# Kernel optimization log

Hardware: AMD Instinct MI355X
Metric: run time of the kernel (lower is better)

## Reference

```python
import jax, jax.numpy as jnp
import numpy as np

B, N, L, H = 32, 1024, 512, 8  # batch, num_id, Input_len, num_head
EPS = 1e-5


def _ln(x, g, b):
    m = jnp.mean(x, axis=-1, keepdims=True)
    v = jnp.mean((x - m) ** 2, axis=-1, keepdims=True)
    return (x - m) / jnp.sqrt(v + EPS) * g + b


def setup_inputs() -> dict:
    key = jax.random.key(0)
    ks = iter(jax.random.split(key, 40))
    w = lambda shape, s=0.02: jax.random.normal(next(ks), shape, jnp.float32) * s
    inp = {"x": jax.random.normal(next(ks), (B, N, L), jnp.float32)}
    for p in ("t", "c"):  # Time_de_att and cross_de_att params (conv1d k=1 -> [L,L])
        inp[f"{p}_Wq"] = w((L, L)); inp[f"{p}_bq"] = w((L,))
        inp[f"{p}_Wk"] = w((L, L)); inp[f"{p}_bk"] = w((L,))
        inp[f"{p}_Wv"] = w((L, L)); inp[f"{p}_bv"] = w((L,))
        inp[f"{p}_Wo"] = w((L, L, 1, H)); inp[f"{p}_bo"] = w((L,))  # Conv2d kernel (1,H)
        inp[f"{p}_g"] = jnp.ones((L,), jnp.float32); inp[f"{p}_b"] = jnp.zeros((L,), jnp.float32)
    inp["s_Wq"] = w((N, N)); inp["s_bq"] = w((N,))
    inp["s_Wk"] = w((N, N)); inp["s_bk"] = w((N,))
    inp["s_Wv"] = w((N, N)); inp["s_bv"] = w((N,))
    inp["s_W1"] = w((1, H)); inp["s_b1"] = w((1,))
    return inp


def _conv1x1(x_cn, W, b):  # x_cn: [B,C,len], W: [O,C]
    return jnp.einsum('oc,bcn->bon', W, x_cn) + b[None, :, None]


def _de_att(xq_src, xkv_src, Wq, bq, Wk, bk, Wv, bv, Wo, bo, g, bt):
    # xq_src, xkv_src: [B,L,N] (channels-first, as after x.transpose(-2,-1))
    q = _conv1x1(xq_src, Wq, bq).transpose(0, 2, 1)   # [B,N,L]
    k = _conv1x1(xkv_src, Wk, bk)                     # [B,L,N]
    v = _conv1x1(xkv_src, Wv, bv).transpose(0, 2, 1)  # [B,N,L]
    kd = jnp.sqrt(jnp.float32(N) / H)                 # k.shape[-1] == num_id
    attn = jax.nn.softmax(jnp.matmul(q, k) / kd, axis=-1)  # [B,N,N]
    line = jnp.matmul(attn, v)                        # [B,N,L]
    # eval-mode: all heads identical -> Conv2d(1,H) combine == sum weights over head axis
    Wsum = Wo[:, :, 0, :].sum(-1)                     # [L,L]
    res = jnp.einsum('oc,bcn->bon', Wsum, line.transpose(0, 2, 1)) + bo[None, :, None]
    out = (xkv_src + res).transpose(0, 2, 1)          # [B,N,L]
    return _ln(out, g, bt)


def reference(x,
              t_Wq, t_bq, t_Wk, t_bk, t_Wv, t_bv, t_Wo, t_bo, t_g, t_b,
              c_Wq, c_bq, c_Wk, c_bk, c_Wv, c_bv, c_Wo, c_bo, c_g, c_b,
              s_Wq, s_bq, s_Wk, s_bk, s_Wv, s_bv, s_W1, s_b1):
    xt = x.transpose(0, 2, 1)  # [B,L,N]
    # Time_de_att (self-attention over nodes, time as channels)
    time_out = _de_att(xt, xt, t_Wq, t_bq, t_Wk, t_bk, t_Wv, t_bv, t_Wo, t_bo, t_g, t_b)  # [B,N,L]
    # space_att2 (attention over time, nodes as features)
    q = xt @ s_Wq.T + s_bq                          # [B,L,N]
    k = (xt @ s_Wk.T + s_bk).transpose(0, 2, 1)     # [B,N,L]
    v = xt @ s_Wv.T + s_bv                          # [B,L,N]
    kd = jnp.sqrt(jnp.float32(L) / H)               # k.shape[-1] == Input_len
    line = jnp.matmul(jax.nn.softmax(jnp.matmul(q, k) / kd, axis=-1), v)  # [B,L,N]
    space_out = (line * s_W1.sum() + s_b1[0]).transpose(0, 2, 1)          # [B,N,L]
    # cross_de_att: q from space_out, k/v + residual from time_out
    out = _de_att(space_out.transpose(0, 2, 1), time_out.transpose(0, 2, 1),
                  c_Wq, c_bq, c_Wk, c_bk, c_Wv, c_bv, c_Wo, c_bo, c_g, c_b)
    return out  # [B,N,L]
```

## Files before the change

kernel.cpp:

```cpp
#include <hip/hip_runtime.h>
#include <hip/hip_bf16.h>

typedef __bf16 bf16;
typedef __bf16 bf16x8 __attribute__((ext_vector_type(8)));
typedef __bf16 bf16x4 __attribute__((ext_vector_type(4)));
typedef __bf16 bf16x2 __attribute__((ext_vector_type(2)));
typedef float f32x4 __attribute__((ext_vector_type(4)));

#define BATCH 32
#define N_ID 1024
#define L_IN 512

static const long ACT_E = (long)BATCH * N_ID * L_IN;
static const long S_NL  = (long)N_ID * L_IN;
static const long S_TT  = (long)N_ID * N_ID;

__device__ __forceinline__ void gload16(const bf16* g, bf16* l)
{
    __builtin_amdgcn_global_load_lds((__attribute__((address_space(1))) void*)g,
                                     (__attribute__((address_space(3))) void*)l, 16, 0, 0);
}

#define VM3 asm volatile("s_waitcnt vmcnt(3)" ::: "memory")
#define VM9 asm volatile("s_waitcnt vmcnt(9)" ::: "memory")
#define VM0 asm volatile("s_waitcnt vmcnt(0)" ::: "memory")
#define BAR __builtin_amdgcn_s_barrier()

#define COMPUTE(CIDX) \
    { \
      const bf16* pa = ldsb + (CIDX) * 12288; \
      const bf16* pb = pa + 8192; \
      bf16x8 af[4], bfv[4]; \
_Pragma("unroll") \
      for (int i = 0; i < 4; ++i) \
        af[i] = *(const bf16x8*)(pa + (wm * 64 + i * 16 + fr) * 32 + slotk); \
_Pragma("unroll") \
      for (int j = 0; j < 4; ++j) \
        bfv[j] = *(const bf16x8*)(pb + (wn * 64 + j * 16 + fr) * 32 + slotk); \
      __builtin_amdgcn_s_setprio(1); \
_Pragma("unroll") \
      for (int i = 0; i < 4; ++i) \
_Pragma("unroll") \
        for (int j = 0; j < 4; ++j) \
          acc[i][j] = __builtin_amdgcn_mfma_f32_16x16x32_bf16(af[i], bfv[j], acc[i][j], 0, 0, 0); \
      __builtin_amdgcn_s_setprio(0); \
    }

#define STAGE(CIDX, KT) { stgA(ldsb + (CIDX) * 12288, KT); \
                          stgB(ldsb + (CIDX) * 12288 + 8192, KT); }

template<int EPI>
__global__ __launch_bounds__(512, 4)
void gemm3(const bf16* __restrict__ A, const bf16* __restrict__ Bm, void* __restrict__ Cout,
           const float* __restrict__ biasCol, const float* __restrict__ biasRow,
           const void* __restrict__ Res, const float* __restrict__ scal2,
           float scale, int K,
           long lda, long ldb, long ldc,
           long sA, long sB, long sC, long sRes, long sBR, long sVp, int nsl,
           unsigned gy, unsigned gxy, unsigned nwg)
{
    __shared__ __align__(16) bf16 ldsbuf[2 * 12288];
    bf16* ldsb = ldsbuf;

    unsigned id = blockIdx.x;
    {
        const unsigned q = nwg >> 3, r = nwg & 7;
        const unsigned xcd = id & 7, off = id >> 3;
        id = (xcd < r ? xcd * (q + 1) : r * (q + 1) + (xcd - r) * q) + off;
    }
    const unsigned bz = id / gxy;
    const unsigned rem = id - bz * gxy;
    const unsigned bx = rem / gy;
    const unsigned by = rem - bx * gy;

    const int t = threadIdx.x;
    const int w = t >> 6;
    const int lane = t & 63;
    const int fr = lane & 15;
    const int kg = lane >> 4;
    const int wm = w >> 1, wn = w & 1;
    const long z = bz;
    const long m0 = (long)bx * 256;
    const long n0 = (long)by * 128;
    const bf16* Ab = A + z * sA;
    const bf16* Bb = Bm + z * sB;

    const int srow = w * 16 + (lane >> 2);
    const int gc = (lane & 3) ^ ((lane >> 3) & 3);
    const int slotk = (kg ^ ((fr >> 1) & 3)) * 8;

    auto stgA = [&](bf16* dst, int kt) {
#pragma unroll
        for (int r = 0; r < 2; ++r) {
            const int row = r * 128 + srow;
            gload16(Ab + (m0 + row) * lda + kt * 32 + gc * 8, dst + row * 32 + (lane & 3) * 8);
        }
    };
    auto stgB = [&](bf16* dst, int kt) {
        gload16(Bb + (n0 + srow) * ldb + kt * 32 + gc * 8, dst + srow * 32 + (lane & 3) * 8);
    };

    f32x4 acc[4][4] = {};

    const int NT = K >> 5;
    STAGE(0, 0); STAGE(1, 1);

    for (int kt = 0; kt < NT - 1; ++kt) {
        VM3; BAR;
        COMPUTE(kt & 1);
        BAR;
        if (kt + 2 < NT) STAGE(kt & 1, kt + 2);
    }
    VM0; BAR;
    COMPUTE((NT - 1) & 1);

    float e0 = 0.f, e1 = 0.f;
    if constexpr (EPI == 8) { e0 = scal2[0]; e1 = scal2[1]; }

    float rs[16];
    if constexpr (EPI == 6) {
#pragma unroll
        for (int vv = 0; vv < 16; ++vv) rs[vv] = 0.f;
    }

#pragma unroll
    for (int i = 0; i < 4; ++i) {
        const long rb = m0 + wm * 64 + i * 16 + kg * 4;
#pragma unroll
        for (int j = 0; j < 4; ++j) {
            const long cc = n0 + wn * 64 + j * 16 + fr;
            float cinv = 0.f, vj = 0.f;
            if constexpr (EPI == 8) {
                float s = 0.f;
#pragma unroll
                for (int k8 = 0; k8 < 8; ++k8) s += biasCol[z * sBR + cc * 8 + k8];
                cinv = 1.f / s;
            }
            if constexpr (EPI == 6) vj = biasCol[z * sVp + cc];
#pragma unroll
            for (int r = 0; r < 4; ++r) {
                const long rr = rb + r;
                const float v = acc[i][j][r];
                const long idx = z * sC + rr * ldc + cc;
                if constexpr (EPI == 1)      ((bf16*)Cout)[idx] = (bf16)(v + biasRow[rr]);
                else if constexpr (EPI == 3) ((bf16*)Cout)[idx] = (bf16)v;
                else if constexpr (EPI == 6) {
                    const float e = __builtin_amdgcn_exp2f(v * scale + vj);
                    ((bf16*)Cout)[idx] = (bf16)e;
                    rs[i * 4 + r] += e;
                }
                else                  ((bf16*)Cout)[idx] = (bf16)(v * cinv * e0 + e1);
            }
        }
    }

    if constexpr (EPI == 6) {
#pragma unroll
        for (int vv = 0; vv < 16; ++vv) {
            rs[vv] += __shfl_xor(rs[vv], 1);
            rs[vv] += __shfl_xor(rs[vv], 2);
            rs[vv] += __shfl_xor(rs[vv], 4);
            rs[vv] += __shfl_xor(rs[vv], 8);
        }
        if (fr == 0) {
            float* Rs = (float*)biasRow + z * sBR;
            const int slot = (int)by * 2 + wn;
#pragma unroll
            for (int i = 0; i < 4; ++i)
#pragma unroll
                for (int r = 0; r < 4; ++r) {
                    const long rr = m0 + wm * 64 + i * 16 + kg * 4 + r;
                    Rs[rr * nsl + slot] = rs[i * 4 + r];
                }
        }
    }
}

template<int OUTF32>
__global__ __launch_bounds__(256, 2)
void pvln(const bf16* __restrict__ P, const bf16* __restrict__ V,
          void* __restrict__ Out,
          const float* __restrict__ biasP, const float* __restrict__ Rslots,
          const bf16* __restrict__ Res,
          const float* __restrict__ g, const float* __restrict__ beta,
          unsigned nwg)
{
    __shared__ __align__(16) bf16 lds[2][18432];
    __shared__ float red[64][4][2];

    unsigned id = blockIdx.x;
    {
        const unsigned q = nwg >> 3, r = nwg & 7;
        const unsigned xcd = id & 7, off = id >> 3;
        id = (xcd < r ? xcd * (q + 1) : r * (q + 1) + (xcd - r) * q) + off;
    }
    const long z = id >> 4;
    const int m0 = (int)(id & 15) * 64;

    const int t = threadIdx.x;
    const int w = t >> 6;
    const int lane = t & 63;
    const int fr = lane & 15;
    const int kg = lane >> 4;

    const bf16* Ab = P + z * S_TT + (long)m0 * 1024;
    const bf16* Bb = V + z * S_NL;

    const int srow = t >> 2;
    const int gc = (t & 3) ^ ((t >> 3) & 3);
    const int slotk = (kg ^ ((fr >> 1) & 3)) * 8;

    auto stg = [&](int buf, int kt) {
        gload16(Ab + (long)srow * 1024 + kt * 32 + gc * 8,
                &lds[buf][srow * 32 + (t & 3) * 8]);
#pragma unroll
        for (int p0 = 0; p0 < 8; ++p0) {
            const int row = p0 * 64 + srow;
            gload16(Bb + (long)row * 1024 + kt * 32 + gc * 8,
                    &lds[buf][2048 + row * 32 + (t & 3) * 8]);
        }
    };

    f32x4 acc[4][8] = {};

    stg(0, 0); stg(1, 1);
#define PVCOMP(CIDX) \
    { \
      const bf16* pa = &lds[CIDX][0]; \
      const bf16* pb = &lds[CIDX][2048]; \
      bf16x8 af[4], bfv[8]; \
_Pragma("unroll") \
      for (int i = 0; i < 4; ++i) \
        af[i] = *(const bf16x8*)(pa + (i * 16 + fr) * 32 + slotk); \
_Pragma("unroll") \
      for (int j = 0; j < 8; ++j) \
        bfv[j] = *(const bf16x8*)(pb + (w * 128 + j * 16 + fr) * 32 + slotk); \
      __builtin_amdgcn_s_setprio(1); \
_Pragma("unroll") \
      for (int i = 0; i < 4; ++i) \
_Pragma("unroll") \
        for (int j = 0; j < 8; ++j) \
          acc[i][j] = __builtin_amdgcn_mfma_f32_16x16x32_bf16(af[i], bfv[j], acc[i][j], 0, 0, 0); \
      __builtin_amdgcn_s_setprio(0); \
    }

    for (int kt = 0; kt < 31; ++kt) {
        VM9; BAR;
        PVCOMP(kt & 1);
        BAR;
        if (kt + 2 < 32) stg(kt & 1, kt + 2);
    }
    VM0; BAR;
    PVCOMP(1);

    float rin[16];
#pragma unroll
    for (int i = 0; i < 4; ++i)
#pragma unroll
        for (int r = 0; r < 4; ++r) {
            float s = Rslots[z * 16384 + (long)(m0 + i * 16 + kg * 4 + r) * 16 + fr];
            s += __shfl_xor(s, 1); s += __shfl_xor(s, 2);
            s += __shfl_xor(s, 4); s += __shfl_xor(s, 8);
            rin[i * 4 + r] = 1.f / s;
        }

    float s1[16] = {}, s2[16] = {};
#pragma unroll
    for (int i = 0; i < 4; ++i)
#pragma unroll
        for (int j = 0; j < 8; ++j) {
            const int col = w * 128 + j * 16 + fr;
            const float bp = biasP[col];
#pragma unroll
            for (int r = 0; r < 4; ++r) {
                const int row = i * 16 + kg * 4 + r;
                float v = acc[i][j][r] * rin[i * 4 + r]
                        + (float)Res[z * S_NL + (long)(m0 + row) * 512 + col] + bp;
                acc[i][j][r] = v;
                s1[i * 4 + r] += v;
                s2[i * 4 + r] += v * v;
            }
        }

#pragma unroll
    for (int vv = 0; vv < 16; ++vv) {
        s1[vv] += __shfl_xor(s1[vv], 1); s2[vv] += __shfl_xor(s2[vv], 1);
        s1[vv] += __shfl_xor(s1[vv], 2); s2[vv] += __shfl_xor(s2[vv], 2);
        s1[vv] += __shfl_xor(s1[vv], 4); s2[vv] += __shfl_xor(s2[vv], 4);
        s1[vv] += __shfl_xor(s1[vv], 8); s2[vv] += __shfl_xor(s2[vv], 8);
    }
    __syncthreads();
    if (fr == 0) {
#pragma unroll
        for (int i = 0; i < 4; ++i)
#pragma unroll
            for (int r = 0; r < 4; ++r) {
                const int row = i * 16 + kg * 4 + r;
                red[row][w][0] = s1[i * 4 + r];
                red[row][w][1] = s2[i * 4 + r];
            }
    }
    __syncthreads();

    float mean[16], rstd[16];
#pragma unroll
    for (int i = 0; i < 4; ++i)
#pragma unroll
        for (int r = 0; r < 4; ++r) {
            const int row = i * 16 + kg * 4 + r;
            const float S1 = red[row][0][0] + red[row][1][0] + red[row][2][0] + red[row][3][0];
            const float S2 = red[row][0][1] + red[row][1][1] + red[row][2][1] + red[row][3][1];
            const float m = S1 * (1.f / 512.f);
            mean[i * 4 + r] = m;
            rstd[i * 4 + r] = rsqrtf(S2 * (1.f / 512.f) - m * m + 1e-5f);
        }

#pragma unroll
    for (int i = 0; i < 4; ++i)
#pragma unroll
        for (int j = 0; j < 8; ++j) {
            const int col = w * 128 + j * 16 + fr;
            const float gg = g[col], bb = beta[col];
#pragma unroll
            for (int r = 0; r < 4; ++r) {
                const int row = i * 16 + kg * 4 + r;
                const float o = (acc[i][j][r] - mean[i * 4 + r]) * rstd[i * 4 + r] * gg + bb;
                const long idx = (z * 1024 + m0 + row) * 512 + col;
                if constexpr (OUTF32) ((float*)Out)[idx] = o;
                else                  ((bf16*)Out)[idx] = (bf16)o;
            }
        }
}

__global__ __launch_bounds__(256)
void transpose_cvt(const float* __restrict__ x, bf16* __restrict__ Xb, bf16* __restrict__ xt)
{
    __shared__ bf16 tile[32][33];
    const int b = blockIdx.z;
    const int n0 = blockIdx.x * 32, l0 = blockIdx.y * 32;
    const long base = (long)b * N_ID * L_IN;
    const int tx = threadIdx.x, ty = threadIdx.y;
#pragma unroll
    for (int i = ty; i < 32; i += 8) {
        const long idx = base + (long)(n0 + i) * L_IN + l0 + tx;
        const bf16 s = (bf16)x[idx];
        Xb[idx] = s;
        tile[i][tx] = s;
    }
    __syncthreads();
#pragma unroll
    for (int i = ty; i < 32; i += 8)
        xt[base + (long)(l0 + i) * N_ID + n0 + tx] = tile[tx][i];
}

struct T6 { const float* s[6]; bf16* d[6]; };

__global__ __launch_bounds__(256)
void transpose512_6(T6 p)
{
    __shared__ bf16 tile[32][33];
    const float* src = p.s[blockIdx.z];
    bf16* dst = p.d[blockIdx.z];
    const int c0 = blockIdx.x * 32, r0 = blockIdx.y * 32;
    const int tx = threadIdx.x, ty = threadIdx.y;
#pragma unroll
    for (int i = ty; i < 32; i += 8)
        tile[i][tx] = (bf16)src[(long)(r0 + i) * 512 + c0 + tx];
    __syncthreads();
#pragma unroll
    for (int i = ty; i < 32; i += 8)
        dst[(long)(c0 + i) * 512 + r0 + tx] = tile[tx][i];
}

template<int N>
__global__ __launch_bounds__(256)
void transpose_mat(const float* __restrict__ a, const float* __restrict__ b,
                   bf16* __restrict__ da, bf16* __restrict__ db)
{
    __shared__ bf16 tile[32][33];
    const float* src = blockIdx.z ? b : a;
    bf16* dst = blockIdx.z ? db : da;
    const int c0 = blockIdx.x * 32, r0 = blockIdx.y * 32;
    const int tx = threadIdx.x, ty = threadIdx.y;
#pragma unroll
    for (int i = ty; i < 32; i += 8)
        tile[i][tx] = (bf16)src[(long)(r0 + i) * N + c0 + tx];
    __syncthreads();
#pragma unroll
    for (int i = ty; i < 32; i += 8)
        dst[(long)(c0 + i) * N + r0 + tx] = tile[tx][i];
}

__global__ void cvt_one(const float* __restrict__ s, bf16* __restrict__ d, int n)
{
    const int i = (blockIdx.x * 256 + threadIdx.x) * 4;
    if (i < n) {
        f32x4 v = *(const f32x4*)(s + i);
        bf16x4 o; o[0] = (bf16)v[0]; o[1] = (bf16)v[1]; o[2] = (bf16)v[2]; o[3] = (bf16)v[3];
        *(bf16x4*)(d + i) = o;
    }
}

__global__ void wo_sum2(const float* __restrict__ a, const float* __restrict__ b,
                        bf16* __restrict__ da, bf16* __restrict__ db)
{
    const int i = blockIdx.x * 256 + threadIdx.x;
    const float* src = blockIdx.y ? b : a;
    bf16* dst = blockIdx.y ? db : da;
    const float* p = src + (long)i * 8;
    float s = 0.f;
#pragma unroll
    for (int h = 0; h < 8; ++h) s += p[h];
    dst[i] = (bf16)s;
}

__global__ __launch_bounds__(64)
void biasfold2(const bf16* __restrict__ WsA, const float* __restrict__ bvA, const float* __restrict__ boA, float* __restrict__ outA,
               const bf16* __restrict__ WsB, const float* __restrict__ bvB, const float* __restrict__ boB, float* __restrict__ outB)
{
    const bf16* Ws = blockIdx.y ? WsB : WsA;
    const float* bv = blockIdx.y ? bvB : bvA;
    const float* bo = blockIdx.y ? boB : boA;
    float* out = blockIdx.y ? outB : outA;
    const int o = blockIdx.x;
    float s = 0.f;
    for (int l = threadIdx.x; l < 512; l += 64)
        s += (float)Ws[(long)o * 512 + l] * bv[l];
#pragma unroll
    for (int off = 32; off > 0; off >>= 1) s += __shfl_xor(s, off);
    if (threadIdx.x == 0) out[o] = bo[o] + s;
}

__global__ __launch_bounds__(64)
void vbarfold(const bf16* WkTrT, const float* tbq, float* vbarT,
              const bf16* WkTrC, const float* cbq, float* vbarC,
              const bf16* sWkTr, const float* sbq, float* vbarS,
              const float* sW1, const float* sb1, float* scal)
{
    const int o = blockIdx.x;
    const int y = blockIdx.y;
    if (y == 3) {
        if (o == 0 && threadIdx.x == 0) {
            float s = 0.f;
            for (int h = 0; h < 8; ++h) s += sW1[h];
            scal[0] = s; scal[1] = sb1[0];
        }
        return;
    }
    const bf16* W; const float* b; float* out; int D;
    if (y == 0)      { if (o >= 512) return; W = WkTrT; b = tbq; out = vbarT; D = 512; }
    else if (y == 1) { if (o >= 512) return; W = WkTrC; b = cbq; out = vbarC; D = 512; }
    else             { W = sWkTr; b = sbq; out = vbarS; D = 1024; }
    float s = 0.f;
    for (int a = threadIdx.x; a < D; a += 64)
        s += (float)W[(long)o * D + a] * b[a];
#pragma unroll
    for (int off = 32; off > 0; off >>= 1) s += __shfl_xor(s, off);
    if (threadIdx.x == 0) out[o] = s;
}

__global__ __launch_bounds__(256)
void vrow2(const bf16* __restrict__ Xb, const float* __restrict__ vbT, float* __restrict__ outT, float scT,
           const bf16* __restrict__ xt, const float* __restrict__ vbS, float* __restrict__ outS, float scS)
{
    const int lane = threadIdx.x & 63;
    if (blockIdx.y == 0) {
        const long row = (long)blockIdx.x * 4 + (threadIdx.x >> 6);
        const bf16* r = Xb + row * 512;
        bf16x8 xv = *(const bf16x8*)(r + lane * 8);
        const float* vb = vbT + lane * 8;
        float s = 0.f;
#pragma unroll
        for (int e = 0; e < 8; ++e) s += (float)xv[e] * vb[e];
#pragma unroll
        for (int o = 32; o > 0; o >>= 1) s += __shfl_xor(s, o);
        if (lane == 0) outT[row] = s * scT;
    } else {
        if (blockIdx.x >= 4096) return;
        const long row = (long)blockIdx.x * 4 + (threadIdx.x >> 6);
        const bf16* r = xt + row * 1024;
        float s = 0.f;
#pragma unroll
        for (int u = 0; u < 2; ++u) {
            bf16x8 xv = *(const bf16x8*)(r + u * 512 + lane * 8);
            const float* vb = vbS + u * 512 + lane * 8;
#pragma unroll
            for (int e = 0; e < 8; ++e) s += (float)xv[e] * vb[e];
        }
#pragma unroll
        for (int o = 32; o > 0; o >>= 1) s += __shfl_xor(s, o);
        if (lane == 0) outS[row] = s * scS;
    }
}

template<int D>
__global__ __launch_bounds__(256)
void vrow(const bf16* __restrict__ Src, const float* __restrict__ vbar,
          float* __restrict__ out, float scale2)
{
    const long row = (long)blockIdx.x * 4 + (threadIdx.x >> 6);
    const int lane = threadIdx.x & 63;
    const bf16* r = Src + row * D;
    float s = 0.f;
#pragma unroll
    for (int u = 0; u < D / 512; ++u) {
        bf16x8 xv = *(const bf16x8*)(r + u * 512 + lane * 8);
        const float* vb = vbar + u * 512 + lane * 8;
#pragma unroll
        for (int e = 0; e < 8; ++e) s += (float)xv[e] * vb[e];
    }
#pragma unroll
    for (int o = 32; o > 0; o >>= 1) s += __shfl_xor(s, o);
    if (lane == 0) out[row] = s * scale2;
}

static void launch_gemm(int epi, const bf16* A, const bf16* B, void* C,
                        const float* bc, const float* br, const void* res, const float* sc2,
                        float scale, int M, int N, int K,
                        long lda, long ldb, long ldc,
                        long sA, long sB, long sC, long sRes, long sBR, long sVp, int nsl,
                        int batches, hipStream_t st)
{
    const unsigned gx = M / 256, gy = N / 128;
    const unsigned gxy = gx * gy, nwg = gxy * (unsigned)batches;
    dim3 g(nwg), blk(512);
    switch (epi) {
    case 1: gemm3<1><<<g, blk, 0, st>>>(A, B, C, bc, br, res, sc2, scale, K, lda, ldb, ldc, sA, sB, sC, sRes, sBR, sVp, nsl, gy, gxy, nwg); break;
    case 3: gemm3<3><<<g, blk, 0, st>>>(A, B, C, bc, br, res, sc2, scale, K, lda, ldb, ldc, sA, sB, sC, sRes, sBR, sVp, nsl, gy, gxy, nwg); break;
    case 6: gemm3<6><<<g, blk, 0, st>>>(A, B, C, bc, br, res, sc2, scale, K, lda, ldb, ldc, sA, sB, sC, sRes, sBR, sVp, nsl, gy, gxy, nwg); break;
    default: gemm3<8><<<g, blk, 0, st>>>(A, B, C, bc, br, res, sc2, scale, K, lda, ldb, ldc, sA, sB, sC, sRes, sBR, sVp, nsl, gy, gxy, nwg); break;
    }
}

extern "C" void kernel_launch(void* const* d_in, const int* in_sizes, int n_in,
                              void* d_out, int out_size, void* d_ws, size_t ws_size,
                              hipStream_t stream)
{
    (void)in_sizes; (void)n_in; (void)out_size;

    const float* x   = (const float*)d_in[0];
    const float* tWq = (const float*)d_in[1];  const float* tbq = (const float*)d_in[2];
    const float* tWk = (const float*)d_in[3];
    const float* tWv = (const float*)d_in[5];  const float* tbv = (const float*)d_in[6];
    const float* tWo = (const float*)d_in[7];  const float* tbo = (const float*)d_in[8];
    const float* tg  = (const float*)d_in[9];  const float* tb  = (const float*)d_in[10];
    const float* cWq = (const float*)d_in[11]; const float* cbq = (const float*)d_in[12];
    const float* cWk = (const float*)d_in[13];
    const float* cWv = (const float*)d_in[15]; const float* cbv = (const float*)d_in[16];
    const float* cWo = (const float*)d_in[17]; const float* cbo = (const float*)d_in[18];
    const float* cg  = (const float*)d_in[19]; const float* cb  = (const float*)d_in[20];
    const float* sWq = (const float*)d_in[21]; const float* sbq = (const float*)d_in[22];
    const float* sWk = (const float*)d_in[23];
    const float* sWv = (const float*)d_in[25]; const float* sbv = (const float*)d_in[26];
    const float* sW1 = (const float*)d_in[27]; const float* sb1 = (const float*)d_in[28];

    char* p = (char*)d_ws;
    auto alloc = [&](size_t bytes) -> char* {
        char* r = p; p += (bytes + 255) & ~(size_t)255; return r;
    };

    bf16* WsT   = (bf16*)alloc(262144 * 2);
    bf16* WsC   = (bf16*)alloc(262144 * 2);
    bf16* WkTrT = (bf16*)alloc(262144 * 2);
    bf16* WkTrC = (bf16*)alloc(262144 * 2);
    bf16* WvTrT = (bf16*)alloc(262144 * 2);
    bf16* WvTrC = (bf16*)alloc(262144 * 2);
    bf16* WqTrT = (bf16*)alloc(262144 * 2);
    bf16* WqTrC = (bf16*)alloc(262144 * 2);
    bf16* WvWT  = (bf16*)alloc(262144 * 2);
    bf16* WvWC  = (bf16*)alloc(262144 * 2);
    bf16* MTt   = (bf16*)alloc(262144 * 2);
    bf16* MTc   = (bf16*)alloc(262144 * 2);
    bf16* sWqTr = (bf16*)alloc(1048576 * 2);
    bf16* sWkTr = (bf16*)alloc(1048576 * 2);
    bf16* MTs   = (bf16*)alloc(1048576 * 2);
    bf16* WvS   = (bf16*)alloc(1048576 * 2);
    float* scal  = (float*)alloc(256);
    float* biasT = (float*)alloc(512 * 4);
    float* biasC = (float*)alloc(512 * 4);
    float* vbarT = (float*)alloc(512 * 4);
    float* vbarC = (float*)alloc(512 * 4);
    float* vbarS = (float*)alloc(1024 * 4);

    const size_t ACT_B = (size_t)ACT_E * 2;
    bf16* bufG = (bf16*)alloc(ACT_B);
    bf16* Xb   = (bf16*)alloc(ACT_B);
    bf16* TO   = (bf16*)alloc(ACT_B);
    bf16* xt   = (bf16*)alloc(ACT_B);
    bf16* bufV = (bf16*)alloc(ACT_B);
    float* vpre = (float*)alloc(BATCH * 1024 * 4);
    float* Rbuf = (float*)alloc((size_t)BATCH * 1024 * 16 * 4);

    size_t used = (size_t)(p - (char*)d_ws);
    int CB = 32;
    while (CB > 1 && used + (size_t)CB * 2097152ULL + 4096 > ws_size) CB >>= 1;
    bf16* Sbuf = (bf16*)alloc((size_t)CB * 2097152ULL);
    bf16* Pbuf = Sbuf;

    const float L2E = 1.4426950408889634f;
    const float rsc_t2 = 0.08838834764831845f * L2E;
    const float rsc_s2 = 0.125f * L2E;

    T6 tj;
    tj.s[0] = tWv; tj.s[1] = cWv; tj.s[2] = tWq; tj.s[3] = cWq; tj.s[4] = tWk; tj.s[5] = cWk;
    tj.d[0] = WvTrT; tj.d[1] = WvTrC; tj.d[2] = WqTrT; tj.d[3] = WqTrC; tj.d[4] = WkTrT; tj.d[5] = WkTrC;
    transpose512_6<<<dim3(16, 16, 6), dim3(32, 8), 0, stream>>>(tj);
    transpose_mat<1024><<<dim3(32, 32, 2), dim3(32, 8), 0, stream>>>(sWq, sWk, sWqTr, sWkTr);
    cvt_one<<<dim3(1024), dim3(256), 0, stream>>>(sWv, WvS, 1048576);
    wo_sum2<<<dim3(1024, 2), dim3(256), 0, stream>>>(tWo, cWo, WsT, WsC);
    biasfold2<<<dim3(512, 2), dim3(64), 0, stream>>>(WsT, tbv, tbo, biasT, WsC, cbv, cbo, biasC);
    vbarfold<<<dim3(1024, 4), dim3(64), 0, stream>>>(WkTrT, tbq, vbarT, WkTrC, cbq, vbarC,
                                                     sWkTr, sbq, vbarS, sW1, sb1, scal);
    launch_gemm(3, WsT, WvTrT, WvWT, nullptr, nullptr, nullptr, nullptr, 0.f,
                512, 512, 512, 512, 512, 512, 262144, 262144, 262144, 0, 0, 0, 0, 4, stream);
    launch_gemm(3, sWkTr, sWqTr, MTs, nullptr, nullptr, nullptr, nullptr, 0.f,
                1024, 1024, 1024, 1024, 1024, 1024, 0, 0, 0, 0, 0, 0, 0, 1, stream);
    transpose_cvt<<<dim3(32, 16, BATCH), dim3(32, 8), 0, stream>>>(x, Xb, xt);
    vrow2<<<dim3(8192, 2), dim3(256), 0, stream>>>(Xb, vbarT, vpre, rsc_t2, xt, vbarS, vpre, rsc_s2);

    launch_gemm(3, Xb, MTt, bufG, nullptr, nullptr, nullptr, nullptr, 0.f,
                32768, 512, 512, 512, 512, 512, 0, 0, 0, 0, 0, 0, 0, 1, stream);
    launch_gemm(3, WvWT, Xb, bufV, nullptr, nullptr, nullptr, nullptr, 0.f,
                512, 1024, 512, 512, 512, 1024, 0, S_NL, S_NL, 0, 0, 0, 0, BATCH, stream);
    for (int c0 = 0; c0 < BATCH; c0 += CB) {
        const long off = (long)c0 * S_NL;
        launch_gemm(6, bufG + off, Xb + off, Sbuf, vpre + (long)c0 * 1024, Rbuf, nullptr, nullptr, rsc_t2,
                    1024, 1024, 512, 512, 512, 1024, S_NL, S_NL, S_TT, 0, 16384, 1024, 16, CB, stream);
        pvln<0><<<dim3(CB * 16), dim3(256), 0, stream>>>(Sbuf, bufV + off, TO + off,
                                                         biasT, Rbuf, Xb + off, tg, tb, CB * 16);
    }

    bf16* SOp = Xb;
    launch_gemm(3, xt, MTs, bufG, nullptr, nullptr, nullptr, nullptr, 0.f,
                16384, 1024, 1024, 1024, 1024, 1024, 0, 0, 0, 0, 0, 0, 0, 1, stream);
    launch_gemm(1, WvS, xt, bufV, nullptr, sbv, nullptr, nullptr, 0.f,
                1024, 512, 1024, 1024, 1024, 512, 0, S_NL, S_NL, 0, 0, 0, 0, BATCH, stream);
    vrow<1024><<<dim3(4096), dim3(256), 0, stream>>>(xt, vbarS, vpre, rsc_s2);
    for (int c0 = 0; c0 < BATCH; c0 += CB) {
        const long off = (long)c0 * S_NL;
        launch_gemm(6, bufG + off, xt + off, Sbuf, vpre + (long)c0 * 512, Rbuf, nullptr, nullptr, rsc_s2,
                    512, 512, 1024, 1024, 1024, 512, S_NL, S_NL, (long)L_IN * L_IN, 0, 4096, 512, 8, CB, stream);
        launch_gemm(8, bufV + off, Pbuf, SOp + off, Rbuf, nullptr, nullptr, scal, 0.f,
                    1024, 512, 512, 512, 512, 512, S_NL, (long)L_IN * L_IN, S_NL, 0, 4096, 0, 8, CB, stream);
    }

    launch_gemm(3, Xb, MTc, bufG, nullptr, nullptr, nullptr, nullptr, 0.f,
                32768, 512, 512, 512, 512, 512, 0, 0, 0, 0, 0, 0, 0, 1, stream);
    launch_gemm(3, WvWC, TO, bufV, nullptr, nullptr, nullptr, nullptr, 0.f,
                512, 1024, 512, 512, 512, 1024, 0, S_NL, S_NL, 0, 0, 0, 0, BATCH, stream);
    vrow<512><<<dim3(8192), dim3(256), 0, stream>>>(TO, vbarC, vpre, rsc_t2);
    for (int c0 = 0; c0 < BATCH; c0 += CB) {
        const long off = (long)c0 * S_NL;
        launch_gemm(6, bufG + off, TO + off, Sbuf, vpre + (long)c0 * 1024, Rbuf, nullptr, nullptr, rsc_t2,
                    1024, 1024, 512, 512, 512, 1024, S_NL, S_NL, S_TT, 0, 16384, 1024, 16, CB, stream);
        pvln<1><<<dim3(CB * 16), dim3(256), 0, stream>>>(Sbuf, bufV + off, (float*)d_out + off,
                                                         biasC, Rbuf, TO + off, cg, cb, CB * 16);
    }
}
```

Baseline: 631.6 us.

## Widen pvln to 512 threads and reuse fused vrow2 output for space pass

```diff
diff --git a/kernel.cpp b/kernel.cpp
--- a/kernel.cpp
+++ b/kernel.cpp
@@ -22,7 +22,6 @@
 }
 
 #define VM3 asm volatile("s_waitcnt vmcnt(3)" ::: "memory")
-#define VM9 asm volatile("s_waitcnt vmcnt(9)" ::: "memory")
 #define VM0 asm volatile("s_waitcnt vmcnt(0)" ::: "memory")
 #define BAR __builtin_amdgcn_s_barrier()
 
@@ -177,7 +176,7 @@
 }
 
 template<int OUTF32>
-__global__ __launch_bounds__(256, 2)
+__global__ __launch_bounds__(512, 2)
 void pvln(const bf16* __restrict__ P, const bf16* __restrict__ V,
           void* __restrict__ Out,
           const float* __restrict__ biasP, const float* __restrict__ Rslots,
@@ -186,7 +185,7 @@
           unsigned nwg)
 {
     __shared__ __align__(16) bf16 lds[2][18432];
-    __shared__ float red[64][4][2];
+    __shared__ float red[64][8][2];
 
     unsigned id = blockIdx.x;
     {
@@ -206,46 +205,51 @@
     const bf16* Ab = P + z * S_TT + (long)m0 * 1024;
     const bf16* Bb = V + z * S_NL;
 
-    const int srow = t >> 2;
+    const int srowB = t >> 2;
     const int gc = (t & 3) ^ ((t >> 3) & 3);
     const int slotk = (kg ^ ((fr >> 1) & 3)) * 8;
 
     auto stg = [&](int buf, int kt) {
-        gload16(Ab + (long)srow * 1024 + kt * 32 + gc * 8,
-                &lds[buf][srow * 32 + (t & 3) * 8]);
-#pragma unroll
-        for (int p0 = 0; p0 < 8; ++p0) {
-            const int row = p0 * 64 + srow;
+        if (t < 256) {
+            const int row = t >> 2;
+            gload16(Ab + (long)row * 1024 + kt * 32 + gc * 8,
+                    &lds[buf][row * 32 + (t & 3) * 8]);
+        }
+#pragma unroll
+        for (int p0 = 0; p0 < 4; ++p0) {
+            const int row = p0 * 128 + srowB;
             gload16(Bb + (long)row * 1024 + kt * 32 + gc * 8,
                     &lds[buf][2048 + row * 32 + (t & 3) * 8]);
         }
     };
 
-    f32x4 acc[4][8] = {};
-
-    stg(0, 0); stg(1, 1);
+    f32x4 acc[4][4] = {};
+
 #define PVCOMP(CIDX) \
     { \
       const bf16* pa = &lds[CIDX][0]; \
       const bf16* pb = &lds[CIDX][2048]; \
-      bf16x8 af[4], bfv[8]; \
+      bf16x8 af[4], bfv[4]; \
 _Pragma("unroll") \
       for (int i = 0; i < 4; ++i) \
         af[i] = *(const bf16x8*)(pa + (i * 16 + fr) * 32 + slotk); \
 _Pragma("unroll") \
-      for (int j = 0; j < 8; ++j) \
-        bfv[j] = *(const bf16x8*)(pb + (w * 128 + j * 16 + fr) * 32 + slotk); \
+      for (int j = 0; j < 4; ++j) \
+        bfv[j] = *(const bf16x8*)(pb + (w * 64 + j * 16 + fr) * 32 + slotk); \
       __builtin_amdgcn_s_setprio(1); \
 _Pragma("unroll") \
       for (int i = 0; i < 4; ++i) \
 _Pragma("unroll") \
-        for (int j = 0; j < 8; ++j) \
+        for (int j = 0; j < 4; ++j) \
           acc[i][j] = __builtin_amdgcn_mfma_f32_16x16x32_bf16(af[i], bfv[j], acc[i][j], 0, 0, 0); \
       __builtin_amdgcn_s_setprio(0); \
     }
 
+    stg(0, 0); stg(1, 1);
     for (int kt = 0; kt < 31; ++kt) {
-        VM9; BAR;
+        if (w < 4) { asm volatile("s_waitcnt vmcnt(5)" ::: "memory"); }
+        else       { asm volatile("s_waitcnt vmcnt(4)" ::: "memory"); }
+        BAR;
         PVCOMP(kt & 1);
         BAR;
         if (kt + 2 < 32) stg(kt & 1, kt + 2);
@@ -268,8 +272,8 @@
 #pragma unroll
     for (int i = 0; i < 4; ++i)
 #pragma unroll
-        for (int j = 0; j < 8; ++j) {
-            const int col = w * 128 + j * 16 + fr;
+        for (int j = 0; j < 4; ++j) {
+            const int col = w * 64 + j * 16 + fr;
             const float bp = biasP[col];
 #pragma unroll
             for (int r = 0; r < 4; ++r) {
@@ -308,8 +312,9 @@
 #pragma unroll
         for (int r = 0; r < 4; ++r) {
             const int row = i * 16 + kg * 4 + r;
-            const float S1 = red[row][0][0] + red[row][1][0] + red[row][2][0] + red[row][3][0];
-            const float S2 = red[row][0][1] + red[row][1][1] + red[row][2][1] + red[row][3][1];
+            float S1 = 0.f, S2 = 0.f;
+#pragma unroll
+            for (int ww = 0; ww < 8; ++ww) { S1 += red[row][ww][0]; S2 += red[row][ww][1]; }
             const float m = S1 * (1.f / 512.f);
             mean[i * 4 + r] = m;
             rstd[i * 4 + r] = rsqrtf(S2 * (1.f / 512.f) - m * m + 1e-5f);
@@ -318,8 +323,8 @@
 #pragma unroll
     for (int i = 0; i < 4; ++i)
 #pragma unroll
-        for (int j = 0; j < 8; ++j) {
-            const int col = w * 128 + j * 16 + fr;
+        for (int j = 0; j < 4; ++j) {
+            const int col = w * 64 + j * 16 + fr;
             const float gg = g[col], bb = beta[col];
 #pragma unroll
             for (int r = 0; r < 4; ++r) {
@@ -588,7 +593,8 @@
     bf16* TO   = (bf16*)alloc(ACT_B);
     bf16* xt   = (bf16*)alloc(ACT_B);
     bf16* bufV = (bf16*)alloc(ACT_B);
-    float* vpre = (float*)alloc(BATCH * 1024 * 4);
+    float* vpreT = (float*)alloc(BATCH * 1024 * 4);
+    float* vpreS = (float*)alloc(BATCH * 512 * 4);
     float* Rbuf = (float*)alloc((size_t)BATCH * 1024 * 16 * 4);
 
     size_t used = (size_t)(p - (char*)d_ws);
@@ -616,7 +622,7 @@
     launch_gemm(3, sWkTr, sWqTr, MTs, nullptr, nullptr, nullptr, nullptr, 0.f,
                 1024, 1024, 1024, 1024, 1024, 1024, 0, 0, 0, 0, 0, 0, 0, 1, stream);
     transpose_cvt<<<dim3(32, 16, BATCH), dim3(32, 8), 0, stream>>>(x, Xb, xt);
-    vrow2<<<dim3(8192, 2), dim3(256), 0, stream>>>(Xb, vbarT, vpre, rsc_t2, xt, vbarS, vpre, rsc_s2);
+    vrow2<<<dim3(8192, 2), dim3(256), 0, stream>>>(Xb, vbarT, vpreT, rsc_t2, xt, vbarS, vpreS, rsc_s2);
 
     launch_gemm(3, Xb, MTt, bufG, nullptr, nullptr, nullptr, nullptr, 0.f,
                 32768, 512, 512, 512, 512, 512, 0, 0, 0, 0, 0, 0, 0, 1, stream);
@@ -624,9 +630,9 @@
                 512, 1024, 512, 512, 512, 1024, 0, S_NL, S_NL, 0, 0, 0, 0, BATCH, stream);
     for (int c0 = 0; c0 < BATCH; c0 += CB) {
         const long off = (long)c0 * S_NL;
-        launch_gemm(6, bufG + off, Xb + off, Sbuf, vpre + (long)c0 * 1024, Rbuf, nullptr, nullptr, rsc_t2,
+        launch_gemm(6, bufG + off, Xb + off, Sbuf, vpreT + (long)c0 * 1024, Rbuf, nullptr, nullptr, rsc_t2,
                     1024, 1024, 512, 512, 512, 1024, S_NL, S_NL, S_TT, 0, 16384, 1024, 16, CB, stream);
-        pvln<0><<<dim3(CB * 16), dim3(256), 0, stream>>>(Sbuf, bufV + off, TO + off,
+        pvln<0><<<dim3(CB * 16), dim3(512), 0, stream>>>(Sbuf, bufV + off, TO + off,
                                                          biasT, Rbuf, Xb + off, tg, tb, CB * 16);
     }
 
@@ -635,10 +641,9 @@
                 16384, 1024, 1024, 1024, 1024, 1024, 0, 0, 0, 0, 0, 0, 0, 1, stream);
     launch_gemm(1, WvS, xt, bufV, nullptr, sbv, nullptr, nullptr, 0.f,
                 1024, 512, 1024, 1024, 1024, 512, 0, S_NL, S_NL, 0, 0, 0, 0, BATCH, stream);
-    vrow<1024><<<dim3(4096), dim3(256), 0, stream>>>(xt, vbarS, vpre, rsc_s2);
     for (int c0 = 0; c0 < BATCH; c0 += CB) {
         const long off = (long)c0 * S_NL;
-        launch_gemm(6, bufG + off, xt + off, Sbuf, vpre + (long)c0 * 512, Rbuf, nullptr, nullptr, rsc_s2,
+        launch_gemm(6, bufG + off, xt + off, Sbuf, vpreS + (long)c0 * 512, Rbuf, nullptr, nullptr, rsc_s2,
                     512, 512, 1024, 1024, 1024, 512, S_NL, S_NL, (long)L_IN * L_IN, 0, 4096, 512, 8, CB, stream);
         launch_gemm(8, bufV + off, Pbuf, SOp + off, Rbuf, nullptr, nullptr, scal, 0.f,
                     1024, 512, 512, 512, 512, 512, S_NL, (long)L_IN * L_IN, S_NL, 0, 4096, 0, 8, CB, stream);
@@ -648,12 +653,12 @@
                 32768, 512, 512, 512, 512, 512, 0, 0, 0, 0, 0, 0, 0, 1, stream);
     launch_gemm(3, WvWC, TO, bufV, nullptr, nullptr, nullptr, nullptr, 0.f,
                 512, 1024, 512, 512, 512, 1024, 0, S_NL, S_NL, 0, 0, 0, 0, BATCH, stream);
-    vrow<512><<<dim3(8192), dim3(256), 0, stream>>>(TO, vbarC, vpre, rsc_t2);
+    vrow<512><<<dim3(8192), dim3(256), 0, stream>>>(TO, vbarC, vpreT, rsc_t2);
     for (int c0 = 0; c0 < BATCH; c0 += CB) {
         const long off = (long)c0 * S_NL;
-        launch_gemm(6, bufG + off, TO + off, Sbuf, vpre + (long)c0 * 1024, Rbuf, nullptr, nullptr, rsc_t2,
+        launch_gemm(6, bufG + off, TO + off, Sbuf, vpreT + (long)c0 * 1024, Rbuf, nullptr, nullptr, rsc_t2,
                     1024, 1024, 512, 512, 512, 1024, S_NL, S_NL, S_TT, 0, 16384, 1024, 16, CB, stream);
-        pvln<1><<<dim3(CB * 16), dim3(256), 0, stream>>>(Sbuf, bufV + off, (float*)d_out + off,
+        pvln<1><<<dim3(CB * 16), dim3(512), 0, stream>>>(Sbuf, bufV + off, (float*)d_out + off,
                                                          biasC, Rbuf, TO + off, cg, cb, CB * 16);
     }
 }
```

New measurement: 651.7 us. +3.2%, slower.
